# Optimization experiments

Hardware: AMD Instinct MI355X
Metric: run time of the kernel (lower is better)

The kernel has to match this reference:

```python
import jax, jax.numpy as jnp
import numpy as np

N = 100000      # num nodes
E = 600000      # num edges
DIN = 64        # input_dim
DH = 128        # hidden_dim
G = 512         # num graphs
EPS = 1e-5      # BatchNorm eps


def setup_inputs() -> dict:
    key = jax.random.key(0)
    ks = jax.random.split(key, 12)
    x = jax.random.normal(ks[0], (N, DIN), jnp.float32)
    edge_index = jax.random.randint(ks[1], (2, E), 0, N)
    batch = jnp.sort(jax.random.randint(ks[2], (N,), 0, G))

    def w(k, shape):
        return (jax.random.normal(k, shape, jnp.float32) / np.float32(np.sqrt(shape[0])))

    inp = {"x": x, "edge_index": edge_index, "batch": batch}
    inp.update(
        W1=w(ks[3], (DIN, DH)), b1=jnp.zeros((DH,), jnp.float32),
        bn1_g=jnp.ones((DH,), jnp.float32), bn1_b=jnp.zeros((DH,), jnp.float32),
        bn1_m=jax.random.normal(ks[4], (DH,), jnp.float32) * 0.1,
        bn1_v=jnp.ones((DH,), jnp.float32),
        W2=w(ks[5], (DH, DH)), b2=jnp.zeros((DH,), jnp.float32),
        bn2_g=jnp.ones((DH,), jnp.float32), bn2_b=jnp.zeros((DH,), jnp.float32),
        bn2_m=jax.random.normal(ks[6], (DH,), jnp.float32) * 0.1,
        bn2_v=jnp.ones((DH,), jnp.float32),
        W3=w(ks[7], (DH, DH)), b3=jnp.zeros((DH,), jnp.float32),
        bn3_g=jnp.ones((DH,), jnp.float32), bn3_b=jnp.zeros((DH,), jnp.float32),
        bn3_m=jax.random.normal(ks[8], (DH,), jnp.float32) * 0.1,
        bn3_v=jnp.ones((DH,), jnp.float32),
        fc1_w=w(ks[9], (DH, DH // 2)), fc1_b=jnp.zeros((DH // 2,), jnp.float32),
        fc2_w=w(ks[10], (DH // 2, 1)), fc2_b=jnp.zeros((1,), jnp.float32),
    )
    return inp


def reference(x, edge_index, batch,
              W1, b1, bn1_g, bn1_b, bn1_m, bn1_v,
              W2, b2, bn2_g, bn2_b, bn2_m, bn2_v,
              W3, b3, bn3_g, bn3_b, bn3_m, bn3_v,
              fc1_w, fc1_b, fc2_w, fc2_b):
    # --- GCN normalization with self-loops (PyG GCNConv, sym norm) ---
    loop = jnp.arange(N, dtype=edge_index.dtype)
    src = jnp.concatenate([edge_index[0], loop])  # [E+N]
    dst = jnp.concatenate([edge_index[1], loop])  # [E+N]
    deg = jax.ops.segment_sum(jnp.ones_like(dst, jnp.float32), dst, num_segments=N)
    dis = jnp.where(deg > 0, jax.lax.rsqrt(jnp.maximum(deg, 1.0)), 0.0)
    norm = (dis[src] * dis[dst])[:, None]  # [E+N, 1]

    def conv(h, W, b):
        h = h @ W
        agg = jax.ops.segment_sum(h[src] * norm, dst, num_segments=N)
        return agg + b

    def bn(h, g, bta, m, v):
        return (h - m) * jax.lax.rsqrt(v + EPS) * g + bta  # eval-mode BatchNorm1d

    # block 1 (dropout is identity in eval)
    h = jax.nn.relu(bn(conv(x, W1, b1), bn1_g, bn1_b, bn1_m, bn1_v))
    # middle residual block (num_layers=3 -> one block)
    h = jax.nn.relu(bn(conv(h, W2, b2), bn2_g, bn2_b, bn2_m, bn2_v)) + h
    # output conv block
    h = jax.nn.relu(bn(conv(h, W3, b3), bn3_g, bn3_b, bn3_m, bn3_v))

    # global mean pool over graphs
    sums = jax.ops.segment_sum(h, batch, num_segments=G)          # [G, DH]
    cnt = jax.ops.segment_sum(jnp.ones((N, 1), h.dtype), batch, num_segments=G)
    pooled = sums / jnp.maximum(cnt, 1.0)

    h = jax.nn.relu(pooled @ fc1_w + fc1_b)
    return jax.nn.sigmoid(h @ fc2_w + fc2_b)  # [G, 1]
```

## Files before the change

### kernel.cpp

```cpp
#include <hip/hip_runtime.h>
#include <math.h>

#define N_NODES 100000
#define N_EDGES 600000
#define DIN     64
#define DH      128
#define NG      512
#define EPS_BN  1e-5f
#define SCAN_TPB 256
#define N_SCAN_BLK ((N_NODES + SCAN_TPB - 1) / SCAN_TPB)
#define G_EDGE   ((N_EDGES + 255) / 256)

typedef unsigned short u16;
typedef short s16x8 __attribute__((ext_vector_type(8)));
typedef float f32x4 __attribute__((ext_vector_type(4)));

__device__ __forceinline__ u16 f2bf(float x) {
    unsigned u = __builtin_bit_cast(unsigned, x);
    u += 0x7fffu + ((u >> 16) & 1u);
    return (u16)(u >> 16);
}
__device__ __forceinline__ float bf2f(u16 h) {
    unsigned u = ((unsigned)h) << 16;
    return __builtin_bit_cast(float, u);
}

#define PREP_WT1_BLKS  32
#define PREP_WT2_BLKS  64
#define PREP_WT3_BLKS  64
#define PREP_BN_BLKS   2
#define PREP_GB_BLKS   3
#define PREP_B0 G_EDGE
#define PREP_B1 (PREP_B0 + PREP_WT1_BLKS)
#define PREP_B2 (PREP_B1 + PREP_WT2_BLKS)
#define PREP_B3 (PREP_B2 + PREP_WT3_BLKS)
#define PREP_B4 (PREP_B3 + PREP_BN_BLKS)
#define PREP_TOTAL (PREP_B4 + PREP_GB_BLKS)

__device__ __forceinline__ void wt_body(const float* __restrict__ W, u16* __restrict__ Wt,
                                        int K, int idx) {
    if (idx >= K * DH) return;
    int k = idx / DH, n = idx % DH;
    Wt[(long)n * K + k] = f2bf(W[idx]);
}

__global__ __launch_bounds__(256) void degprep_kernel(
    const int* __restrict__ dst, int* __restrict__ deg,
    const float* __restrict__ W1, u16* __restrict__ Wt1,
    const float* __restrict__ W2, u16* __restrict__ Wt2,
    const float* __restrict__ W3, u16* __restrict__ Wt3,
    const float* b1, const float* g1, const float* bb1, const float* m1, const float* v1,
    const float* b2, const float* g2, const float* bb2, const float* m2, const float* v2,
    const float* b3, const float* g3, const float* bb3, const float* m3, const float* v3,
    float* __restrict__ sc, float* __restrict__ sh,
    const int* __restrict__ batch, int* __restrict__ gp) {
    const int b = blockIdx.x;
    const int tid = threadIdx.x;
    if (b < PREP_B0) {
        const int e = b * 256 + tid;
        if (e < N_EDGES) atomicAdd(&deg[dst[e]], 1);
    } else if (b < PREP_B1) {
        wt_body(W1, Wt1, DIN, (b - PREP_B0) * 256 + tid);
    } else if (b < PREP_B2) {
        wt_body(W2, Wt2, DH, (b - PREP_B1) * 256 + tid);
    } else if (b < PREP_B3) {
        wt_body(W3, Wt3, DH, (b - PREP_B2) * 256 + tid);
    } else if (b < PREP_B4) {
        const int i = (b - PREP_B3) * 256 + tid;
        if (i < 3 * DH) {
            int l = i >> 7, c = i & (DH - 1);
            const float* bc = l == 0 ? b1 : (l == 1 ? b2 : b3);
            const float* g  = l == 0 ? g1 : (l == 1 ? g2 : g3);
            const float* bb = l == 0 ? bb1 : (l == 1 ? bb2 : bb3);
            const float* m  = l == 0 ? m1 : (l == 1 ? m2 : m3);
            const float* v  = l == 0 ? v1 : (l == 1 ? v2 : v3);
            float s = g[c] * rsqrtf(v[c] + EPS_BN);
            sc[i] = s;
            sh[i] = (bc[c] - m[c]) * s + bb[c];
        }
    } else {
        const int g = (b - PREP_B4) * 256 + tid;
        if (g <= NG) {
            int lo = 0, hi = N_NODES;
            while (lo < hi) {
                int mid = (lo + hi) >> 1;
                if (batch[mid] < g) lo = mid + 1; else hi = mid;
            }
            gp[g] = lo;
        }
    }
}

__global__ __launch_bounds__(SCAN_TPB) void scan1_kernel(const int* __restrict__ deg,
                                                         float* __restrict__ dis,
                                                         int* __restrict__ rp,
                                                         int* __restrict__ blk, int n) {
    __shared__ int sm[SCAN_TPB];
    const int t = threadIdx.x;
    const int i = blockIdx.x * SCAN_TPB + t;
    int v = 0;
    if (i < n) {
        v = deg[i];
        dis[i] = rsqrtf((float)v + 1.0f);
    }
    sm[t] = v;
    __syncthreads();
#pragma unroll
    for (int off = 1; off < SCAN_TPB; off <<= 1) {
        int u = (t >= off) ? sm[t - off] : 0;
        __syncthreads();
        sm[t] += u;
        __syncthreads();
    }
    if (i <= n) rp[i] = sm[t] - v;
    if (t == SCAN_TPB - 1) blk[blockIdx.x] = sm[t];
}

__global__ __launch_bounds__(512) void scan2_kernel(int* __restrict__ blk, int nblk) {
    __shared__ int sm[512];
    const int t = threadIdx.x;
    const int v = (t < nblk) ? blk[t] : 0;
    sm[t] = v;
    __syncthreads();
#pragma unroll
    for (int off = 1; off < 512; off <<= 1) {
        int u = (t >= off) ? sm[t - off] : 0;
        __syncthreads();
        sm[t] += u;
        __syncthreads();
    }
    if (t < nblk) blk[t] = sm[t] - v;
}

__global__ __launch_bounds__(256) void build_csr_kernel(const int* __restrict__ src,
                                                        const int* __restrict__ dst,
                                                        const int* __restrict__ rp,
                                                        const int* __restrict__ blk,
                                                        int* __restrict__ cursor,
                                                        int* __restrict__ col, int E) {
    int e = blockIdx.x * blockDim.x + threadIdx.x;
    if (e >= E) return;
    const int s = src[e];
    const int d = dst[e];
    const int p = atomicAdd(&cursor[d], 1);
    col[rp[d] + blk[d >> 8] + p] = s;
}

template <int K, bool AF32>
__global__ __launch_bounds__(256) void gemm_mfma(const void* __restrict__ Ain,
                                                 const u16* __restrict__ Wt,
                                                 const float* __restrict__ dis,
                                                 u16* __restrict__ C,
                                                 int M) {
    __shared__ u16 ldsc[4][16][DH];
    const int wave = threadIdx.x >> 6;
    const int lane = threadIdx.x & 63;
    const int r16 = lane & 15;
    const int kc  = lane >> 4;
    const long row0 = (long)blockIdx.x * 64 + wave * 16;

    f32x4 acc[8];
#pragma unroll
    for (int t = 0; t < 8; ++t)
#pragma unroll
        for (int q = 0; q < 4; ++q) acc[t][q] = 0.0f;

    long arow = row0 + r16;
    if (arow >= M) arow = M - 1;

#pragma unroll
    for (int ks = 0; ks < K; ks += 32) {
        s16x8 a;
        if constexpr (AF32) {
            const float* ap = (const float*)Ain + arow * K + ks + kc * 8;
            const float4 f0 = *(const float4*)(ap);
            const float4 f1 = *(const float4*)(ap + 4);
            a[0] = (short)f2bf(f0.x); a[1] = (short)f2bf(f0.y);
            a[2] = (short)f2bf(f0.z); a[3] = (short)f2bf(f0.w);
            a[4] = (short)f2bf(f1.x); a[5] = (short)f2bf(f1.y);
            a[6] = (short)f2bf(f1.z); a[7] = (short)f2bf(f1.w);
        } else {
            a = *(const s16x8*)((const u16*)Ain + arow * K + ks + kc * 8);
        }
#pragma unroll
        for (int t = 0; t < 8; ++t) {
            const s16x8 b = *(const s16x8*)(Wt + (long)(t * 16 + r16) * K + ks + kc * 8);
            acc[t] = __builtin_amdgcn_mfma_f32_16x16x32_bf16(a, b, acc[t], 0, 0, 0);
        }
    }

    float dd[4];
#pragma unroll
    for (int q = 0; q < 4; ++q) {
        long r = row0 + kc * 4 + q;
        dd[q] = dis[r < M ? r : (M - 1)];
    }

#pragma unroll
    for (int t = 0; t < 8; ++t) {
        const int blkc = (t << 1) | (r16 >> 3);
        const int co = r16 & 7;
#pragma unroll
        for (int q = 0; q < 4; ++q) {
            const int row = kc * 4 + q;
            ldsc[wave][row][(((blkc ^ (row & 7)) << 3) | co)] = f2bf(acc[t][q] * dd[q]);
        }
    }
#pragma unroll
    for (int it = 0; it < 4; ++it) {
        const int rl = (lane >> 4) + it * 4;
        const long row = row0 + rl;
        if (row < M) {
            const int phys = (lane & 15) ^ (rl & 7);
            const s16x8 v = *(const s16x8*)&ldsc[wave][rl][phys << 3];
            *(s16x8*)(C + row * DH + ((lane & 15) << 3)) = v;
        }
    }
}

template <bool RES>
__global__ __launch_bounds__(256) void agg_epi_kernel(const u16* __restrict__ H,
                                                      const int* __restrict__ rp,
                                                      const int* __restrict__ blk,
                                                      const int* __restrict__ col,
                                                      const float* __restrict__ dis,
                                                      const float* __restrict__ scl,
                                                      const float* __restrict__ shf,
                                                      u16* __restrict__ out, int n) {
    const long t = (long)blockIdx.x * blockDim.x + threadIdx.x;
    const int lane = (int)(t & 31);
    const long i = t >> 5;
    if (i >= n) return;
    const int cl = lane & 15;
    const int eh = lane >> 4;
    const int c = cl * 8;

    float acc[8] = {0, 0, 0, 0, 0, 0, 0, 0};
    if (eh == 0) {
        const s16x8 hv = *(const s16x8*)(H + i * DH + c);
#pragma unroll
        for (int q = 0; q < 8; ++q) acc[q] = bf2f((u16)hv[q]);
    }

    const int beg = rp[i] + blk[i >> 8];
    const int end = rp[i + 1] + blk[(int)(i + 1) >> 8];
    for (int e = beg + eh; e < end; e += 2) {
        const int s = col[e];
        const s16x8 v = *(const s16x8*)(H + (long)s * DH + c);
#pragma unroll
        for (int q = 0; q < 8; ++q) acc[q] += bf2f((u16)v[q]);
    }

#pragma unroll
    for (int q = 0; q < 8; ++q) acc[q] += __shfl_xor(acc[q], 16);

    if (eh == 0) {
        const float dd = dis[i];
        const float4 s0 = *(const float4*)(scl + c);
        const float4 s1 = *(const float4*)(scl + c + 4);
        const float4 f0 = *(const float4*)(shf + c);
        const float4 f1 = *(const float4*)(shf + c + 4);
        const float sv[8] = {s0.x, s0.y, s0.z, s0.w, s1.x, s1.y, s1.z, s1.w};
        const float fv[8] = {f0.x, f0.y, f0.z, f0.w, f1.x, f1.y, f1.z, f1.w};

        float r[8];
#pragma unroll
        for (int q = 0; q < 8; ++q) r[q] = fmaxf(fmaf(acc[q] * dd, sv[q], fv[q]), 0.0f);
        if (RES) {
            const s16x8 rv = *(const s16x8*)(out + i * DH + c);
#pragma unroll
            for (int q = 0; q < 8; ++q) r[q] += bf2f((u16)rv[q]);
        }
        s16x8 ov;
#pragma unroll
        for (int q = 0; q < 8; ++q) ov[q] = (short)f2bf(r[q]);
        __builtin_nontemporal_store(ov, (s16x8*)(out + i * DH + c));
    }
}

__global__ __launch_bounds__(256) void pool_head_kernel(const u16* __restrict__ h,
                                                        const int* __restrict__ gp,
                                                        const float* __restrict__ fc1w,
                                                        const float* __restrict__ fc1b,
                                                        const float* __restrict__ fc2w,
                                                        const float* __restrict__ fc2b,
                                                        float* __restrict__ out) {
    const int g = blockIdx.x;
    const int t = threadIdx.x;
    const int grp = t >> 4;
    const int cl = t & 15;
    const int c = cl * 8;
    const int beg = gp[g];
    const int end = gp[g + 1];

    float acc[8] = {0, 0, 0, 0, 0, 0, 0, 0};
    for (int i = beg + grp; i < end; i += 16) {
        const s16x8 v = *(const s16x8*)(h + (long)i * DH + c);
#pragma unroll
        for (int q = 0; q < 8; ++q) acc[q] += bf2f((u16)v[q]);
    }

    __shared__ float sm[16][DH];
    __shared__ float p[DH];
#pragma unroll
    for (int q = 0; q < 8; ++q) sm[grp][c + q] = acc[q];
    __syncthreads();

    if (t < DH) {
        float s = 0.0f;
#pragma unroll
        for (int r = 0; r < 16; ++r) s += sm[r][t];
        p[t] = s / fmaxf((float)(end - beg), 1.0f);
    }
    __syncthreads();

    if (t < 64) {
        float a = 0.0f;
#pragma unroll 4
        for (int k = 0; k < DH; ++k) a = fmaf(p[k], fc1w[(long)k * 64 + t], a);
        const float h1 = fmaxf(a + fc1b[t], 0.0f);
        float v = h1 * fc2w[t];
#pragma unroll
        for (int off = 32; off > 0; off >>= 1) v += __shfl_down(v, off);
        if (t == 0) out[g] = 1.0f / (1.0f + expf(-(v + fc2b[0])));
    }
}

extern "C" void kernel_launch(void* const* d_in, const int* in_sizes, int n_in,
                              void* d_out, int out_size, void* d_ws, size_t ws_size,
                              hipStream_t stream) {
    const float* x     = (const float*)d_in[0];
    const int*   ei    = (const int*)d_in[1];
    const int*   batch = (const int*)d_in[2];
    const float* W1 = (const float*)d_in[3];
    const float* b1 = (const float*)d_in[4];
    const float* g1 = (const float*)d_in[5];
    const float* t1 = (const float*)d_in[6];
    const float* m1 = (const float*)d_in[7];
    const float* v1 = (const float*)d_in[8];
    const float* W2 = (const float*)d_in[9];
    const float* b2 = (const float*)d_in[10];
    const float* g2 = (const float*)d_in[11];
    const float* t2 = (const float*)d_in[12];
    const float* m2 = (const float*)d_in[13];
    const float* v2 = (const float*)d_in[14];
    const float* W3 = (const float*)d_in[15];
    const float* b3 = (const float*)d_in[16];
    const float* g3 = (const float*)d_in[17];
    const float* t3 = (const float*)d_in[18];
    const float* m3 = (const float*)d_in[19];
    const float* v3 = (const float*)d_in[20];
    const float* fc1w = (const float*)d_in[21];
    const float* fc1b = (const float*)d_in[22];
    const float* fc2w = (const float*)d_in[23];
    const float* fc2b = (const float*)d_in[24];

    const int* src = ei;
    const int* dst = ei + N_EDGES;

    char* ws = (char*)d_ws;
    size_t off = 0;
    auto alloc = [&](size_t bytes) -> char* {
        char* p = ws + off;
        off = (off + bytes + 511) & ~(size_t)511;
        return p;
    };
    int*   deg     = (int*)  alloc((size_t)2 * N_NODES * 4);
    int*   cursor  = deg + N_NODES;
    float* dis     = (float*)alloc((size_t)N_NODES * 4);
    int*   rp      = (int*)  alloc(((size_t)N_NODES + 1) * 4);
    int*   blk     = (int*)  alloc((size_t)N_SCAN_BLK * 4);
    int*   col     = (int*)  alloc((size_t)N_EDGES * 4);
    int*   gp      = (int*)  alloc((size_t)(NG + 1) * 4);
    float* bnsc    = (float*)alloc((size_t)3 * DH * 4);
    float* bnsh    = (float*)alloc((size_t)3 * DH * 4);
    u16*   Wt1     = (u16*)  alloc((size_t)DH * DIN * 2);
    u16*   Wt2     = (u16*)  alloc((size_t)DH * DH * 2);
    u16*   Wt3     = (u16*)  alloc((size_t)DH * DH * 2);
    u16*   bufB    = (u16*)  alloc((size_t)N_NODES * DH * 2);
    u16*   bufA    = (u16*)  alloc((size_t)N_NODES * DH * 2);

    const int TPB = 256;
    const int gGemm = (N_NODES + 63) / 64;
    const int gAgg  = (int)(((long)N_NODES * 32 + TPB - 1) / TPB);

    hipMemsetAsync(deg, 0, (size_t)2 * N_NODES * 4, stream);
    degprep_kernel<<<PREP_TOTAL, TPB, 0, stream>>>(dst, deg, W1, Wt1, W2, Wt2, W3, Wt3,
                                                   b1, g1, t1, m1, v1,
                                                   b2, g2, t2, m2, v2,
                                                   b3, g3, t3, m3, v3,
                                                   bnsc, bnsh, batch, gp);
    scan1_kernel<<<N_SCAN_BLK, SCAN_TPB, 0, stream>>>(deg, dis, rp, blk, N_NODES);
    scan2_kernel<<<1, 512, 0, stream>>>(blk, N_SCAN_BLK);
    build_csr_kernel<<<G_EDGE, TPB, 0, stream>>>(src, dst, rp, blk, cursor, col, N_EDGES);

    gemm_mfma<DIN, true><<<gGemm, TPB, 0, stream>>>((const void*)x, Wt1, dis, bufB,
                                                    N_NODES);
    agg_epi_kernel<false><<<gAgg, TPB, 0, stream>>>(bufB, rp, blk, col, dis,
                                                    bnsc, bnsh, bufA, N_NODES);
    gemm_mfma<DH, false><<<gGemm, TPB, 0, stream>>>((const void*)bufA, Wt2, dis, bufB,
                                                    N_NODES);
    agg_epi_kernel<true><<<gAgg, TPB, 0, stream>>>(bufB, rp, blk, col, dis,
                                                   bnsc + DH, bnsh + DH, bufA, N_NODES);
    gemm_mfma<DH, false><<<gGemm, TPB, 0, stream>>>((const void*)bufA, Wt3, dis, bufB,
                                                    N_NODES);
    agg_epi_kernel<false><<<gAgg, TPB, 0, stream>>>(bufB, rp, blk, col, dis,
                                                    bnsc + 2 * DH, bnsh + 2 * DH, bufA,
                                                    N_NODES);

    pool_head_kernel<<<NG, TPB, 0, stream>>>(bufA, gp, fc1w, fc1b, fc2w, fc2b,
                                             (float*)d_out);
}
```

Measured before the change: 289.9 us.

## Aggregate layer-1 input before GEMM using 64-wide features and fuse BN epilogue

Layer 1 is reordered to aggregate first and transform second (A·X·W). The x-to-bf16 conversion with the dis pre-scale is merged into the CSR-build launch, a new 64-channel gather kernel aggregates the narrower input features, and the first GEMM then applies bias, BatchNorm and ReLU in its epilogue. This halves the gathered bytes for the first sparse aggregation and removes one 128-wide aggregation pass. The cost is an extra 64-wide intermediate buffer and an extra kernel, and the output now uses bf16 rounding of x before aggregation.

Result: faster. 280.6 us (-3.2%).

```diff
diff --git a/kernel.cpp b/kernel.cpp
--- a/kernel.cpp
+++ b/kernel.cpp
@@ -132,24 +132,90 @@
     if (t < nblk) blk[t] = sm[t] - v;
 }
 
-__global__ __launch_bounds__(256) void build_csr_kernel(const int* __restrict__ src,
-                                                        const int* __restrict__ dst,
-                                                        const int* __restrict__ rp,
-                                                        const int* __restrict__ blk,
-                                                        int* __restrict__ cursor,
-                                                        int* __restrict__ col, int E) {
-    int e = blockIdx.x * blockDim.x + threadIdx.x;
-    if (e >= E) return;
-    const int s = src[e];
-    const int d = dst[e];
-    const int p = atomicAdd(&cursor[d], 1);
-    col[rp[d] + blk[d >> 8] + p] = s;
-}
-
-template <int K, bool AF32>
-__global__ __launch_bounds__(256) void gemm_mfma(const void* __restrict__ Ain,
+#define CSRX_XCVT_BLKS 3125
+#define CSRX_TOTAL (G_EDGE + CSRX_XCVT_BLKS)
+__global__ __launch_bounds__(256) void csr_xcvt_kernel(const int* __restrict__ src,
+                                                       const int* __restrict__ dst,
+                                                       const int* __restrict__ rp,
+                                                       const int* __restrict__ blk,
+                                                       int* __restrict__ cursor,
+                                                       int* __restrict__ col,
+                                                       const float* __restrict__ x,
+                                                       const float* __restrict__ dis,
+                                                       u16* __restrict__ xb) {
+    const int b = blockIdx.x;
+    const int tid = threadIdx.x;
+    if (b < G_EDGE) {
+        const int e = b * 256 + tid;
+        if (e >= N_EDGES) return;
+        const int s = src[e];
+        const int d = dst[e];
+        const int p = atomicAdd(&cursor[d], 1);
+        col[rp[d] + blk[d >> 8] + p] = s;
+    } else {
+        const long base = ((long)(b - G_EDGE) * 256 + tid) * 8;
+        const float dd = dis[base >> 6];
+        const float4 a = *(const float4*)(x + base);
+        const float4 c = *(const float4*)(x + base + 4);
+        s16x8 o;
+        o[0] = (short)f2bf(a.x * dd); o[1] = (short)f2bf(a.y * dd);
+        o[2] = (short)f2bf(a.z * dd); o[3] = (short)f2bf(a.w * dd);
+        o[4] = (short)f2bf(c.x * dd); o[5] = (short)f2bf(c.y * dd);
+        o[6] = (short)f2bf(c.z * dd); o[7] = (short)f2bf(c.w * dd);
+        *(s16x8*)(xb + base) = o;
+    }
+}
+
+__global__ __launch_bounds__(256) void agg64_kernel(const u16* __restrict__ xb,
+                                                    const int* __restrict__ rp,
+                                                    const int* __restrict__ blk,
+                                                    const int* __restrict__ col,
+                                                    const float* __restrict__ dis,
+                                                    u16* __restrict__ aggX, int n) {
+    const long t = (long)blockIdx.x * blockDim.x + threadIdx.x;
+    const int lane = (int)(t & 31);
+    const long i = t >> 5;
+    if (i >= n) return;
+    const int cl = lane & 7;
+    const int eh = (lane >> 3) & 3;
+    const int c = cl * 8;
+
+    float acc[8] = {0, 0, 0, 0, 0, 0, 0, 0};
+    if (eh == 0) {
+        const s16x8 hv = *(const s16x8*)(xb + i * DIN + c);
+#pragma unroll
+        for (int q = 0; q < 8; ++q) acc[q] = bf2f((u16)hv[q]);
+    }
+
+    const int beg = rp[i] + blk[i >> 8];
+    const int end = rp[i + 1] + blk[(int)(i + 1) >> 8];
+    for (int e = beg + eh; e < end; e += 4) {
+        const int s = col[e];
+        const s16x8 v = *(const s16x8*)(xb + (long)s * DIN + c);
+#pragma unroll
+        for (int q = 0; q < 8; ++q) acc[q] += bf2f((u16)v[q]);
+    }
+
+#pragma unroll
+    for (int q = 0; q < 8; ++q) acc[q] += __shfl_xor(acc[q], 8);
+#pragma unroll
+    for (int q = 0; q < 8; ++q) acc[q] += __shfl_xor(acc[q], 16);
+
+    if (eh == 0 && (lane >> 4) == 0) {
+        const float dd = dis[i];
+        s16x8 ov;
+#pragma unroll
+        for (int q = 0; q < 8; ++q) ov[q] = (short)f2bf(acc[q] * dd);
+        *(s16x8*)(aggX + i * DIN + c) = ov;
+    }
+}
+
+template <int K, bool BN_EPI>
+__global__ __launch_bounds__(256) void gemm_mfma(const u16* __restrict__ A,
                                                  const u16* __restrict__ Wt,
                                                  const float* __restrict__ dis,
+                                                 const float* __restrict__ scl,
+                                                 const float* __restrict__ shf,
                                                  u16* __restrict__ C,
                                                  int M) {
     __shared__ u16 ldsc[4][16][DH];
@@ -170,18 +236,7 @@
 
 #pragma unroll
     for (int ks = 0; ks < K; ks += 32) {
-        s16x8 a;
-        if constexpr (AF32) {
-            const float* ap = (const float*)Ain + arow * K + ks + kc * 8;
-            const float4 f0 = *(const float4*)(ap);
-            const float4 f1 = *(const float4*)(ap + 4);
-            a[0] = (short)f2bf(f0.x); a[1] = (short)f2bf(f0.y);
-            a[2] = (short)f2bf(f0.z); a[3] = (short)f2bf(f0.w);
-            a[4] = (short)f2bf(f1.x); a[5] = (short)f2bf(f1.y);
-            a[6] = (short)f2bf(f1.z); a[7] = (short)f2bf(f1.w);
-        } else {
-            a = *(const s16x8*)((const u16*)Ain + arow * K + ks + kc * 8);
-        }
+        const s16x8 a = *(const s16x8*)(A + arow * K + ks + kc * 8);
 #pragma unroll
         for (int t = 0; t < 8; ++t) {
             const s16x8 b = *(const s16x8*)(Wt + (long)(t * 16 + r16) * K + ks + kc * 8);
@@ -189,11 +244,19 @@
         }
     }
 
-    float dd[4];
-#pragma unroll
-    for (int q = 0; q < 4; ++q) {
-        long r = row0 + kc * 4 + q;
-        dd[q] = dis[r < M ? r : (M - 1)];
+    float dd[4], scv[8], shv[8];
+    if constexpr (BN_EPI) {
+#pragma unroll
+        for (int t = 0; t < 8; ++t) {
+            scv[t] = scl[t * 16 + r16];
+            shv[t] = shf[t * 16 + r16];
+        }
+    } else {
+#pragma unroll
+        for (int q = 0; q < 4; ++q) {
+            long r = row0 + kc * 4 + q;
+            dd[q] = dis[r < M ? r : (M - 1)];
+        }
     }
 
 #pragma unroll
@@ -203,7 +266,13 @@
 #pragma unroll
         for (int q = 0; q < 4; ++q) {
             const int row = kc * 4 + q;
-            ldsc[wave][row][(((blkc ^ (row & 7)) << 3) | co)] = f2bf(acc[t][q] * dd[q]);
+            float y;
+            if constexpr (BN_EPI) {
+                y = fmaxf(fmaf(acc[t][q], scv[t], shv[t]), 0.0f);
+            } else {
+                y = acc[t][q] * dd[q];
+            }
+            ldsc[wave][row][(((blkc ^ (row & 7)) << 3) | co)] = f2bf(y);
         }
     }
 #pragma unroll
@@ -377,6 +446,8 @@
     u16*   Wt1     = (u16*)  alloc((size_t)DH * DIN * 2);
     u16*   Wt2     = (u16*)  alloc((size_t)DH * DH * 2);
     u16*   Wt3     = (u16*)  alloc((size_t)DH * DH * 2);
+    u16*   xb      = (u16*)  alloc((size_t)N_NODES * DIN * 2);
+    u16*   aggX    = (u16*)  alloc((size_t)N_NODES * DIN * 2);
     u16*   bufB    = (u16*)  alloc((size_t)N_NODES * DH * 2);
     u16*   bufA    = (u16*)  alloc((size_t)N_NODES * DH * 2);
 
@@ -392,17 +463,17 @@
                                                    bnsc, bnsh, batch, gp);
     scan1_kernel<<<N_SCAN_BLK, SCAN_TPB, 0, stream>>>(deg, dis, rp, blk, N_NODES);
     scan2_kernel<<<1, 512, 0, stream>>>(blk, N_SCAN_BLK);
-    build_csr_kernel<<<G_EDGE, TPB, 0, stream>>>(src, dst, rp, blk, cursor, col, N_EDGES);
-
-    gemm_mfma<DIN, true><<<gGemm, TPB, 0, stream>>>((const void*)x, Wt1, dis, bufB,
+    csr_xcvt_kernel<<<CSRX_TOTAL, TPB, 0, stream>>>(src, dst, rp, blk, cursor, col,
+                                                    x, dis, xb);
+
+    agg64_kernel<<<gAgg, TPB, 0, stream>>>(xb, rp, blk, col, dis, aggX, N_NODES);
+    gemm_mfma<DIN, true><<<gGemm, TPB, 0, stream>>>(aggX, Wt1, dis, bnsc, bnsh, bufA,
                                                     N_NODES);
-    agg_epi_kernel<false><<<gAgg, TPB, 0, stream>>>(bufB, rp, blk, col, dis,
-                                                    bnsc, bnsh, bufA, N_NODES);
-    gemm_mfma<DH, false><<<gGemm, TPB, 0, stream>>>((const void*)bufA, Wt2, dis, bufB,
+    gemm_mfma<DH, false><<<gGemm, TPB, 0, stream>>>(bufA, Wt2, dis, bnsc, bnsh, bufB,
                                                     N_NODES);
     agg_epi_kernel<true><<<gAgg, TPB, 0, stream>>>(bufB, rp, blk, col, dis,
                                                    bnsc + DH, bnsh + DH, bufA, N_NODES);
-    gemm_mfma<DH, false><<<gGemm, TPB, 0, stream>>>((const void*)bufA, Wt3, dis, bufB,
+    gemm_mfma<DH, false><<<gGemm, TPB, 0, stream>>>(bufA, Wt3, dis, bnsc, bnsh, bufB,
                                                     N_NODES);
     agg_epi_kernel<false><<<gAgg, TPB, 0, stream>>>(bufB, rp, blk, col, dis,
                                                     bnsc + 2 * DH, bnsh + 2 * DH, bufA,
```
